# Performance work log

Hardware: AMD Instinct MI355X
Metric: run time of the kernel (lower is better)

The kernel has to match this reference:

```python
import jax, jax.numpy as jnp
import numpy as np

B, F, H, N, S = 1024, 256, 256, 128, 2
DEV_MIN, DEV_MAX = 0.001, 0.01
LOG2PI = float(np.log(2.0 * np.pi))  # k/2*log(2pi) with k=2


def setup_inputs() -> dict:
    key = jax.random.key(0)
    ks = jax.random.split(key, 16)
    d = {}
    d['latents'] = jax.random.normal(ks[0], (B, F), jnp.float32)
    d['realPoints'] = jax.random.uniform(ks[1], (B, 2), jnp.float32)
    d['predMu'] = jax.random.uniform(ks[2], (B, 2), jnp.float32)
    d['predScale'] = 0.01 + 0.05 * jax.random.uniform(ks[3], (B, 2), jnp.float32)
    d['eps'] = jax.random.normal(ks[4], (S, B * N, 2), jnp.float32)
    dims = [F] + [H] * 5
    for i in range(5):
        d[f'W{i}'] = jax.random.normal(ks[5 + i], (dims[i], dims[i + 1]), jnp.float32) / np.sqrt(dims[i])
        d[f'b{i}'] = jnp.zeros((dims[i + 1],), jnp.float32)
    d['Wp'] = jax.random.normal(ks[10], (N, H, 2), jnp.float32) / np.sqrt(H)
    d['bp'] = jnp.zeros((N, 2), jnp.float32)
    return d


def _mvn_logprob(x, mu, s):
    # diagonal 2D Gaussian log_prob; broadcasts over leading dims
    z = (x - mu) / s
    return -0.5 * jnp.sum(z * z, axis=-1) - jnp.sum(jnp.log(s), axis=-1) - LOG2PI


def reference(latents, realPoints, predMu, predScale, eps,
              W0, b0, W1, b1, W2, b2, W3, b3, W4, b4, Wp, bp):
    h = latents
    for W, b in ((W0, b0), (W1, b1), (W2, b2), (W3, b3), (W4, b4)):
        h = jax.nn.relu(h @ W + b)
    mu = 0.5 + jnp.einsum('bh,nhk->bnk', h, Wp) + bp          # (B, N, 2)
    Bn, Nn = mu.shape[0], mu.shape[1]
    dev = jnp.linspace(DEV_MIN, DEV_MAX, Nn)[:, None]          # (N, 1)
    scale = jnp.tile(dev, (Bn, 2))                             # (B*N, 2)
    muF = mu.reshape(Bn * Nn, 2)

    # real-points loss: log_prob of each real point under all N gaussians, sigmoid
    pts_real = jnp.repeat(realPoints, Nn, axis=0)              # (B*N, 2)
    realLoss = jax.nn.sigmoid(_mvn_logprob(pts_real, muF, scale).reshape(Bn, Nn))

    # reparameterized samples: (S, B*N, 2) -> (S*N, B, 2)
    sampled = muF + scale * eps
    sampled = sampled.reshape(S, Bn, Nn, 2).transpose(0, 2, 1, 3).reshape(S * Nn, Bn, 2)

    # discriminator lossA: log_prob under detached predicted dist, sigmoid(-x), MSLE vs 0.5
    pmD = jax.lax.stop_gradient(predMu)
    psD = jax.lax.stop_gradient(predScale)
    la = _mvn_logprob(sampled, pmD, psD)                       # (S*N, B)
    la = la.reshape(S, Nn, Bn).transpose(2, 1, 0)              # (B, N, S)
    la = jax.nn.sigmoid(-la)
    lossA = jnp.mean(jnp.square(jnp.log1p(0.5) - jnp.log1p(la)), axis=-1)  # (B, N)

    # discriminator lossB: all-pairs log_prob of samples under own gaussians
    # equivalent to tf.repeat(sampled, N, axis=-2) then log_prob against (B*N,) batch
    z = (sampled[:, :, None, :] - mu[None, :, :, :]) / dev     # (S*N, B, N, 2)
    lb = -0.5 * jnp.sum(z * z, axis=-1) - 2.0 * jnp.log(dev[:, 0]) - LOG2PI  # (S*N, B, N)
    lb = lb.reshape(S, Nn, Bn, Nn).transpose(2, 1, 0, 3)       # (B, N, S, N)
    sm = jax.nn.softmax(lb, axis=-1)
    idx = jnp.arange(Nn)[None, :, None, None]
    diag = jnp.take_along_axis(sm, idx, axis=-1)[..., 0]       # (B, N, S)
    lossB = jnp.square(1.0 - diag)

    # generator loss: log_prob of detached samples under (non-detached) predicted dist
    gl = _mvn_logprob(jax.lax.stop_gradient(sampled), predMu, predScale)  # (S*N, B)
    gl = jax.nn.sigmoid(gl).reshape(S, Nn, Bn).transpose(2, 1, 0)
    gl = jnp.mean(gl, axis=-1)                                 # (B, N)
    genLoss = gl * jax.lax.stop_gradient(1.0 - realLoss)

    return (sampled, genLoss, realLoss, lossA, lossB)
```

## Files before the change

kernel.cpp:

```cpp
#include <hip/hip_runtime.h>
#include <math.h>

#define BB   1024
#define HH   256
#define NN   128
#define SS   2
#define RR   4
#define LOG2PI_F 1.8378770664093453f
#define DEV_MIN_F 0.001f
#define DEV_STEP_F 7.08661417322835e-05f
#define LOG1P_HALF 0.40546510810816438f
#define SHIFT_F 12.0f

#define OFF_GEN  524288
#define OFF_REAL 655360
#define OFF_A    786432
#define OFF_B    917504

typedef float f4_t __attribute__((ext_vector_type(4)));

#define FMA4(ACC, HS, WV)                                         \
    {                                                             \
        ACC.x = fmaf(HS, WV.x, ACC.x);                            \
        ACC.y = fmaf(HS, WV.y, ACC.y);                            \
        ACC.z = fmaf(HS, WV.z, ACC.z);                            \
        ACC.w = fmaf(HS, WV.w, ACC.w);                            \
    }

#define BAR_LGKM() asm volatile("s_waitcnt lgkmcnt(0)\n\ts_barrier" ::: "memory")

__global__ __launch_bounds__(256) void transpose_wp_kernel(
    const float* __restrict__ Wp, float* __restrict__ Wt) {
    const int t = threadIdx.x;
    const int k = blockIdx.x * 2 + (t >> 7);
    const int n = t & 127;
    const float2 v = ((const float2*)Wp)[n * 256 + k];
    *(float2*)&Wt[k * 256 + 2 * n] = v;
}

__global__ __launch_bounds__(1024, 4) void mlp_loss_kernel(
    const float* __restrict__ latents, const float* __restrict__ eps,
    const float* __restrict__ realPts, const float* __restrict__ predMu,
    const float* __restrict__ predScale,
    const float* __restrict__ W0, const float* __restrict__ b0,
    const float* __restrict__ W1, const float* __restrict__ b1,
    const float* __restrict__ W2, const float* __restrict__ b2,
    const float* __restrict__ W3, const float* __restrict__ b3,
    const float* __restrict__ W4, const float* __restrict__ b4,
    const float* __restrict__ Wt, const float* __restrict__ bp,
    float* __restrict__ out) {
    __shared__ __align__(16) float hb[RR][256];
    __shared__ __align__(16) float part[16][RR][256];
    __shared__ float2 sprm[NN];

    const int t  = threadIdx.x;
    const int q  = t >> 6;
    const int c  = t & 63;
    const int rL = t >> 8;
    const int j  = t & 255;
    const int brow = blockIdx.x * RR;

    if (t < NN) {
        float dv = DEV_MIN_F + (float)t * DEV_STEP_F;
        sprm[t] = make_float2(-0.5f / (dv * dv), -2.f * __logf(dv) - LOG2PI_F);
    }
    hb[rL][j] = latents[(brow + rL) * 256 + j];

    float biasv[6];
    biasv[0] = b0[j]; biasv[1] = b1[j]; biasv[2] = b2[j];
    biasv[3] = b3[j]; biasv[4] = b4[j]; biasv[5] = bp[j];

    const int nL = j >> 1, sL = j & 1;
    const int b = brow + rL;
    const float2 epv = ((const float2*)eps)[sL * (BB * NN) + b * NN + nL];

    const float* Wsrc[6] = {W0, W1, W2, W3, W4, Wt};
    const int woff = (q * 16) * 256 + 4 * c;

    f4_t wpa, wpb, wpc, wpd;
    {
        const float* Wn = W0 + woff;
        wpa = *(const f4_t*)(Wn + 0 * 256);
        wpb = *(const f4_t*)(Wn + 1 * 256);
        wpc = *(const f4_t*)(Wn + 2 * 256);
        wpd = *(const f4_t*)(Wn + 3 * 256);
    }

    BAR_LGKM();

    #pragma unroll
    for (int L = 0; L < 6; ++L) {
        const float* __restrict__ Wb = Wsrc[L] + woff;
        f4_t acc[4];
        #pragma unroll
        for (int r = 0; r < 4; ++r) acc[r] = (f4_t)0.f;

        {
            const int kb = q * 16;
            #pragma unroll
            for (int r = 0; r < 4; ++r) {
                f4_t hv = *(const f4_t*)&hb[r][kb];
                FMA4(acc[r], hv.x, wpa);
                FMA4(acc[r], hv.y, wpb);
                FMA4(acc[r], hv.z, wpc);
                FMA4(acc[r], hv.w, wpd);
            }
        }

        #pragma unroll
        for (int i = 1; i < 4; ++i) {
            f4_t w0 = *(const f4_t*)(Wb + (i * 4 + 0) * 256);
            f4_t w1 = *(const f4_t*)(Wb + (i * 4 + 1) * 256);
            f4_t w2 = *(const f4_t*)(Wb + (i * 4 + 2) * 256);
            f4_t w3 = *(const f4_t*)(Wb + (i * 4 + 3) * 256);
            const int kb = q * 16 + i * 4;
            #pragma unroll
            for (int r = 0; r < 4; ++r) {
                f4_t hv = *(const f4_t*)&hb[r][kb];
                FMA4(acc[r], hv.x, w0);
                FMA4(acc[r], hv.y, w1);
                FMA4(acc[r], hv.z, w2);
                FMA4(acc[r], hv.w, w3);
            }
        }

        if (L < 5) {
            const float* Wn = Wsrc[L + 1] + woff;
            wpa = *(const f4_t*)(Wn + 0 * 256);
            wpb = *(const f4_t*)(Wn + 1 * 256);
            wpc = *(const f4_t*)(Wn + 2 * 256);
            wpd = *(const f4_t*)(Wn + 3 * 256);
        }

        #pragma unroll
        for (int r = 0; r < 4; ++r)
            *(f4_t*)&part[q][r][4 * c] = acc[r];
        BAR_LGKM();

        float v0 = part[0][rL][j]  + part[1][rL][j]  + part[2][rL][j]  + part[3][rL][j];
        float v1 = part[4][rL][j]  + part[5][rL][j]  + part[6][rL][j]  + part[7][rL][j];
        float v2 = part[8][rL][j]  + part[9][rL][j]  + part[10][rL][j] + part[11][rL][j];
        float v3 = part[12][rL][j] + part[13][rL][j] + part[14][rL][j] + part[15][rL][j];
        float val = (v0 + v1) + (v2 + v3);
        val += biasv[L];
        if (L == 5) val += 0.5f;
        else        val = fmaxf(val, 0.f);
        hb[rL][j] = val;
        BAR_LGKM();
    }

    const float* __restrict__ muL = &hb[rL][0];
    const int n = nL, s = sL;
    const float devn = DEV_MIN_F + (float)n * DEV_STEP_F;
    const float2 prn = sprm[n];

    const float mux = muL[2 * n], muy = muL[2 * n + 1];
    const float px = fmaf(devn, epv.x, mux);
    const float py = fmaf(devn, epv.y, muy);

    ((float2*)out)[(size_t)(s * NN + n) * BB + b] = make_float2(px, py);

    const float2 pm = ((const float2*)predMu)[b];
    const float2 ps = ((const float2*)predScale)[b];
    const float2 rp = ((const float2*)realPts)[b];

    float PX0 = px,              PY0 = py;
    float PX1 = __shfl_xor(px, 1), PY1 = __shfl_xor(py, 1);
    float PX2 = __shfl_xor(px, 2), PY2 = __shfl_xor(py, 2);
    float PX3 = __shfl_xor(px, 3), PY3 = __shfl_xor(py, 3);

    const int me = t & 3;
    float S0 = 0.f, S1 = 0.f, S2 = 0.f, S3 = 0.f;
    #pragma unroll 4
    for (int mi = 0; mi < 16; ++mi) {
        f4_t mm = *(const f4_t*)&muL[16 * mi + 4 * me];
        f4_t pr = *(const f4_t*)((const float*)sprm + 16 * mi + 4 * me);
        float dx, dy, lb;
        dx = PX0 - mm.x; dy = PY0 - mm.y;
        lb = fmaf(fmaf(dx, dx, dy * dy), pr.x, pr.y); S0 += __expf(lb - SHIFT_F);
        dx = PX1 - mm.x; dy = PY1 - mm.y;
        lb = fmaf(fmaf(dx, dx, dy * dy), pr.x, pr.y); S1 += __expf(lb - SHIFT_F);
        dx = PX2 - mm.x; dy = PY2 - mm.y;
        lb = fmaf(fmaf(dx, dx, dy * dy), pr.x, pr.y); S2 += __expf(lb - SHIFT_F);
        dx = PX3 - mm.x; dy = PY3 - mm.y;
        lb = fmaf(fmaf(dx, dx, dy * dy), pr.x, pr.y); S3 += __expf(lb - SHIFT_F);
        dx = PX0 - mm.z; dy = PY0 - mm.w;
        lb = fmaf(fmaf(dx, dx, dy * dy), pr.z, pr.w); S0 += __expf(lb - SHIFT_F);
        dx = PX1 - mm.z; dy = PY1 - mm.w;
        lb = fmaf(fmaf(dx, dx, dy * dy), pr.z, pr.w); S1 += __expf(lb - SHIFT_F);
        dx = PX2 - mm.z; dy = PY2 - mm.w;
        lb = fmaf(fmaf(dx, dx, dy * dy), pr.z, pr.w); S2 += __expf(lb - SHIFT_F);
        dx = PX3 - mm.z; dy = PY3 - mm.w;
        lb = fmaf(fmaf(dx, dx, dy * dy), pr.z, pr.w); S3 += __expf(lb - SHIFT_F);
    }
    float sum = S0 + __shfl_xor(S1, 1) + __shfl_xor(S2, 2) + __shfl_xor(S3, 3);
    (void)me;

    float dxd = devn * epv.x, dyd = devn * epv.y;
    float lbd = fmaf(fmaf(dxd, dxd, dyd * dyd), prn.x, prn.y);
    float ed  = __expf(lbd - SHIFT_F);
    float diag = ed / sum;
    float lbv = (1.f - diag) * (1.f - diag);
    out[OFF_B + (size_t)b * (NN * SS) + j] = lbv;

    float zx = (px - pm.x) / ps.x, zy = (py - pm.y) / ps.y;
    float la = -0.5f * (zx * zx + zy * zy) - __logf(ps.x) - __logf(ps.y) - LOG2PI_F;
    float aa = 1.f / (1.f + __expf(la));
    float termA = LOG1P_HALF - log1pf(aa);
    termA = termA * termA;
    float gg = 1.f / (1.f + __expf(-la));

    float drx = rp.x - mux, dry = rp.y - muy;
    float lr = fmaf(fmaf(drx, drx, dry * dry), prn.x, prn.y);
    float rl = 1.f / (1.f + __expf(-lr));

    float termA_sum = termA + __shfl_xor(termA, 1);
    float gg_sum    = gg + __shfl_xor(gg, 1);
    if (s == 0) {
        out[OFF_GEN  + (size_t)b * NN + n] = 0.5f * gg_sum * (1.f - rl);
        out[OFF_REAL + (size_t)b * NN + n] = rl;
        out[OFF_A    + (size_t)b * NN + n] = 0.5f * termA_sum;
    }
}

extern "C" void kernel_launch(void* const* d_in, const int* in_sizes, int n_in,
                              void* d_out, int out_size, void* d_ws, size_t ws_size,
                              hipStream_t stream) {
    const float* latents   = (const float*)d_in[0];
    const float* realPts   = (const float*)d_in[1];
    const float* predMu    = (const float*)d_in[2];
    const float* predScale = (const float*)d_in[3];
    const float* eps       = (const float*)d_in[4];
    const float* W0 = (const float*)d_in[5];
    const float* b0 = (const float*)d_in[6];
    const float* W1 = (const float*)d_in[7];
    const float* b1 = (const float*)d_in[8];
    const float* W2 = (const float*)d_in[9];
    const float* b2 = (const float*)d_in[10];
    const float* W3 = (const float*)d_in[11];
    const float* b3 = (const float*)d_in[12];
    const float* W4 = (const float*)d_in[13];
    const float* b4 = (const float*)d_in[14];
    const float* Wp = (const float*)d_in[15];
    const float* bp = (const float*)d_in[16];

    float* Wtp = (float*)d_ws;

    transpose_wp_kernel<<<dim3(128), dim3(256), 0, stream>>>(Wp, Wtp);
    mlp_loss_kernel<<<dim3(BB / RR), dim3(1024), 0, stream>>>(
        latents, eps, realPts, predMu, predScale,
        W0, b0, W1, b1, W2, b2, W3, b3, W4, b4, Wtp, bp, (float*)d_out);
}
```

Before: 116.0 us.

## Stage sample stores through LDS, preload layer weights, use native exp2/log2

The sampled points are staged in shared memory, so each output row is written as 16-byte chunks of four consecutive batch entries instead of scattered 8-byte stores with a stride of BB. All 12 remaining weight vectors of each layer are loaded into registers up front, and the next layer's prefetch is issued before the FMAs to expose more memory-level parallelism. Exponentials and logs are moved to base 2 using native exp2/log2 builtins, with the shift folded into the precomputed parameters, and one sigmoid is derived from the other. This raises register pressure under launch_bounds(1024,4) and adds an extra barrier at the end.

```diff
diff --git a/kernel.cpp b/kernel.cpp
--- a/kernel.cpp
+++ b/kernel.cpp
@@ -11,6 +11,10 @@
 #define DEV_STEP_F 7.08661417322835e-05f
 #define LOG1P_HALF 0.40546510810816438f
 #define SHIFT_F 12.0f
+#define L2E_F       1.4426950408889634f
+#define SHIFT_L2E_F 17.312340490667561f
+#define NHALF_L2E_F -0.7213475204444817f
+#define LOG2PI_L2E_F 2.6514961294723187f
 
 #define OFF_GEN  524288
 #define OFF_REAL 655360
@@ -28,6 +32,21 @@
     }
 
 #define BAR_LGKM() asm volatile("s_waitcnt lgkmcnt(0)\n\ts_barrier" ::: "memory")
+
+__device__ __forceinline__ float fast_exp2(float x) {
+#if __has_builtin(__builtin_amdgcn_exp2f)
+    return __builtin_amdgcn_exp2f(x);
+#else
+    return exp2f(x);
+#endif
+}
+__device__ __forceinline__ float fast_log2(float x) {
+#if __has_builtin(__builtin_amdgcn_logf)
+    return __builtin_amdgcn_logf(x);
+#else
+    return log2f(x);
+#endif
+}
 
 __global__ __launch_bounds__(256) void transpose_wp_kernel(
     const float* __restrict__ Wp, float* __restrict__ Wt) {
@@ -62,7 +81,9 @@
 
     if (t < NN) {
         float dv = DEV_MIN_F + (float)t * DEV_STEP_F;
-        sprm[t] = make_float2(-0.5f / (dv * dv), -2.f * __logf(dv) - LOG2PI_F);
+        float a  = -0.5f / (dv * dv);
+        float bb_ = fmaf(-2.f, __logf(dv), -LOG2PI_F);
+        sprm[t] = make_float2(a * L2E_F, (bb_ - SHIFT_F) * L2E_F);
     }
     hb[rL][j] = latents[(brow + rL) * 256 + j];
 
@@ -91,6 +112,12 @@
     #pragma unroll
     for (int L = 0; L < 6; ++L) {
         const float* __restrict__ Wb = Wsrc[L] + woff;
+
+        f4_t w[12];
+        #pragma unroll
+        for (int u = 0; u < 12; ++u)
+            w[u] = *(const f4_t*)(Wb + (4 + u) * 256);
+
         f4_t acc[4];
         #pragma unroll
         for (int r = 0; r < 4; ++r) acc[r] = (f4_t)0.f;
@@ -107,29 +134,25 @@
             }
         }
 
-        #pragma unroll
-        for (int i = 1; i < 4; ++i) {
-            f4_t w0 = *(const f4_t*)(Wb + (i * 4 + 0) * 256);
-            f4_t w1 = *(const f4_t*)(Wb + (i * 4 + 1) * 256);
-            f4_t w2 = *(const f4_t*)(Wb + (i * 4 + 2) * 256);
-            f4_t w3 = *(const f4_t*)(Wb + (i * 4 + 3) * 256);
-            const int kb = q * 16 + i * 4;
-            #pragma unroll
-            for (int r = 0; r < 4; ++r) {
-                f4_t hv = *(const f4_t*)&hb[r][kb];
-                FMA4(acc[r], hv.x, w0);
-                FMA4(acc[r], hv.y, w1);
-                FMA4(acc[r], hv.z, w2);
-                FMA4(acc[r], hv.w, w3);
-            }
-        }
-
         if (L < 5) {
             const float* Wn = Wsrc[L + 1] + woff;
             wpa = *(const f4_t*)(Wn + 0 * 256);
             wpb = *(const f4_t*)(Wn + 1 * 256);
             wpc = *(const f4_t*)(Wn + 2 * 256);
             wpd = *(const f4_t*)(Wn + 3 * 256);
+        }
+
+        #pragma unroll
+        for (int i = 1; i < 4; ++i) {
+            const int kb = q * 16 + i * 4;
+            #pragma unroll
+            for (int r = 0; r < 4; ++r) {
+                f4_t hv = *(const f4_t*)&hb[r][kb];
+                FMA4(acc[r], hv.x, w[(i - 1) * 4 + 0]);
+                FMA4(acc[r], hv.y, w[(i - 1) * 4 + 1]);
+                FMA4(acc[r], hv.z, w[(i - 1) * 4 + 2]);
+                FMA4(acc[r], hv.w, w[(i - 1) * 4 + 3]);
+            }
         }
 
         #pragma unroll
@@ -158,13 +181,14 @@
     const float px = fmaf(devn, epv.x, mux);
     const float py = fmaf(devn, epv.y, muy);
 
-    ((float2*)out)[(size_t)(s * NN + n) * BB + b] = make_float2(px, py);
+    float2* samp = (float2*)&part[0][0][0];
+    samp[(s * NN + n) * RR + rL] = make_float2(px, py);
 
     const float2 pm = ((const float2*)predMu)[b];
     const float2 ps = ((const float2*)predScale)[b];
     const float2 rp = ((const float2*)realPts)[b];
 
-    float PX0 = px,              PY0 = py;
+    float PX0 = px,                PY0 = py;
     float PX1 = __shfl_xor(px, 1), PY1 = __shfl_xor(py, 1);
     float PX2 = __shfl_xor(px, 2), PY2 = __shfl_xor(py, 2);
     float PX3 = __shfl_xor(px, 3), PY3 = __shfl_xor(py, 3);
@@ -175,44 +199,43 @@
     for (int mi = 0; mi < 16; ++mi) {
         f4_t mm = *(const f4_t*)&muL[16 * mi + 4 * me];
         f4_t pr = *(const f4_t*)((const float*)sprm + 16 * mi + 4 * me);
-        float dx, dy, lb;
+        float dx, dy;
         dx = PX0 - mm.x; dy = PY0 - mm.y;
-        lb = fmaf(fmaf(dx, dx, dy * dy), pr.x, pr.y); S0 += __expf(lb - SHIFT_F);
+        S0 += fast_exp2(fmaf(fmaf(dx, dx, dy * dy), pr.x, pr.y));
         dx = PX1 - mm.x; dy = PY1 - mm.y;
-        lb = fmaf(fmaf(dx, dx, dy * dy), pr.x, pr.y); S1 += __expf(lb - SHIFT_F);
+        S1 += fast_exp2(fmaf(fmaf(dx, dx, dy * dy), pr.x, pr.y));
         dx = PX2 - mm.x; dy = PY2 - mm.y;
-        lb = fmaf(fmaf(dx, dx, dy * dy), pr.x, pr.y); S2 += __expf(lb - SHIFT_F);
+        S2 += fast_exp2(fmaf(fmaf(dx, dx, dy * dy), pr.x, pr.y));
         dx = PX3 - mm.x; dy = PY3 - mm.y;
-        lb = fmaf(fmaf(dx, dx, dy * dy), pr.x, pr.y); S3 += __expf(lb - SHIFT_F);
+        S3 += fast_exp2(fmaf(fmaf(dx, dx, dy * dy), pr.x, pr.y));
         dx = PX0 - mm.z; dy = PY0 - mm.w;
-        lb = fmaf(fmaf(dx, dx, dy * dy), pr.z, pr.w); S0 += __expf(lb - SHIFT_F);
+        S0 += fast_exp2(fmaf(fmaf(dx, dx, dy * dy), pr.z, pr.w));
         dx = PX1 - mm.z; dy = PY1 - mm.w;
-        lb = fmaf(fmaf(dx, dx, dy * dy), pr.z, pr.w); S1 += __expf(lb - SHIFT_F);
+        S1 += fast_exp2(fmaf(fmaf(dx, dx, dy * dy), pr.z, pr.w));
         dx = PX2 - mm.z; dy = PY2 - mm.w;
-        lb = fmaf(fmaf(dx, dx, dy * dy), pr.z, pr.w); S2 += __expf(lb - SHIFT_F);
+        S2 += fast_exp2(fmaf(fmaf(dx, dx, dy * dy), pr.z, pr.w));
         dx = PX3 - mm.z; dy = PY3 - mm.w;
-        lb = fmaf(fmaf(dx, dx, dy * dy), pr.z, pr.w); S3 += __expf(lb - SHIFT_F);
+        S3 += fast_exp2(fmaf(fmaf(dx, dx, dy * dy), pr.z, pr.w));
     }
     float sum = S0 + __shfl_xor(S1, 1) + __shfl_xor(S2, 2) + __shfl_xor(S3, 3);
-    (void)me;
 
     float dxd = devn * epv.x, dyd = devn * epv.y;
-    float lbd = fmaf(fmaf(dxd, dxd, dyd * dyd), prn.x, prn.y);
-    float ed  = __expf(lbd - SHIFT_F);
+    float ed  = fast_exp2(fmaf(fmaf(dxd, dxd, dyd * dyd), prn.x, prn.y));
     float diag = ed / sum;
     float lbv = (1.f - diag) * (1.f - diag);
     out[OFF_B + (size_t)b * (NN * SS) + j] = lbv;
 
     float zx = (px - pm.x) / ps.x, zy = (py - pm.y) / ps.y;
-    float la = -0.5f * (zx * zx + zy * zy) - __logf(ps.x) - __logf(ps.y) - LOG2PI_F;
-    float aa = 1.f / (1.f + __expf(la));
+    float la2 = fmaf(fmaf(zx, zx, zy * zy), NHALF_L2E_F,
+                     -(fast_log2(ps.x) + fast_log2(ps.y)) - LOG2PI_L2E_F);
+    float aa = 1.f / (1.f + fast_exp2(la2));
+    float gg = 1.f - aa;
     float termA = LOG1P_HALF - log1pf(aa);
     termA = termA * termA;
-    float gg = 1.f / (1.f + __expf(-la));
 
     float drx = rp.x - mux, dry = rp.y - muy;
-    float lr = fmaf(fmaf(drx, drx, dry * dry), prn.x, prn.y);
-    float rl = 1.f / (1.f + __expf(-lr));
+    float lr2 = fmaf(fmaf(drx, drx, dry * dry), prn.x, prn.y);
+    float rl = 1.f / (1.f + fast_exp2(-lr2 - SHIFT_L2E_F));
 
     float termA_sum = termA + __shfl_xor(termA, 1);
     float gg_sum    = gg + __shfl_xor(gg, 1);
@@ -220,6 +243,13 @@
         out[OFF_GEN  + (size_t)b * NN + n] = 0.5f * gg_sum * (1.f - rl);
         out[OFF_REAL + (size_t)b * NN + n] = rl;
         out[OFF_A    + (size_t)b * NN + n] = 0.5f * termA_sum;
+    }
+
+    BAR_LGKM();
+    if (t < 512) {
+        const int sn = t >> 1, rp2 = t & 1;
+        f4_t v = *(const f4_t*)&samp[sn * RR + rp2 * 2];
+        *(f4_t*)&((float2*)out)[(size_t)sn * BB + brow + rp2 * 2] = v;
     }
 }
 
```

New measurement: 115.6 us. Within noise of the previous version (-0.4%).
